# Performance work log

Hardware: AMD Instinct MI355X
Metric: run time of the kernel (lower is better)

Reference implementation:

```python
import jax, jax.numpy as jnp
import numpy as np

D = 1024
H = 16
DH = D // H  # 64
EPS = 1e-6


def setup_inputs() -> dict:
    key = jax.random.key(0)
    ks = jax.random.split(key, 12)
    B, Nq, Nk = 4, 2048, 2048
    s = 1.0 / np.sqrt(D)
    return {
        "x": jax.random.normal(ks[0], (B, Nq, D), dtype=jnp.float32),
        "context": jax.random.normal(ks[1], (B, Nk, D), dtype=jnp.float32),
        "Wq": jax.random.normal(ks[2], (D, D), dtype=jnp.float32) * s,
        "bq": jnp.zeros((D,), dtype=jnp.float32),
        "Wk": jax.random.normal(ks[3], (D, D), dtype=jnp.float32) * s,
        "bk": jnp.zeros((D,), dtype=jnp.float32),
        "Wv": jax.random.normal(ks[4], (D, D), dtype=jnp.float32) * s,
        "bv": jnp.zeros((D,), dtype=jnp.float32),
        "Wo": jax.random.normal(ks[5], (D, D), dtype=jnp.float32) * s,
        "bo": jnp.zeros((D,), dtype=jnp.float32),
    }


def _split_heads(t):
    B, N, _ = t.shape
    return t.reshape(B, N, H, DH).transpose(0, 2, 1, 3)  # (B,H,N,DH)


def reference(x, context, Wq, bq, Wk, bk, Wv, bv, Wo, bo):
    B, Nq, _ = x.shape
    # QKV projections (torch Linear: x @ W.T + b)
    q = _split_heads(x @ Wq.T + bq)          # (B,H,Nq,DH)
    k = _split_heads(context @ Wk.T + bk)    # (B,H,Nk,DH)
    v = _split_heads(context @ Wv.T + bv)    # (B,H,Nk,DH)
    # QK-norm (use_qk_norm=True), scale buffer = 1.0
    q = q / (jnp.linalg.norm(q, axis=-1, keepdims=True) + EPS)
    k = k / (jnp.linalg.norm(k, axis=-1, keepdims=True) + EPS)
    scale = jnp.float32(1.0)
    attn = jnp.einsum("bhqd,bhkd->bhqk", q, k) * scale
    attn = jax.nn.softmax(attn, axis=-1)
    out = jnp.einsum("bhqk,bhkd->bhqd", attn, v)  # (B,H,Nq,DH)
    out = out.transpose(0, 2, 1, 3).reshape(B, Nq, D)
    return out @ Wo.T + bo
```

## Files before the change

### kernel.cpp

```cpp
#include <hip/hip_runtime.h>

typedef unsigned short u16;
typedef unsigned int u32;
typedef __attribute__((ext_vector_type(8))) short bf16x8;
typedef __attribute__((ext_vector_type(4))) float f32x4;
typedef __attribute__((ext_vector_type(16))) float f32x16;
typedef __attribute__((ext_vector_type(4))) u32 u32x4;

#define D_MODEL 1024
#define NHEAD 16
#define DHEAD 64
#define SEQ 2048
#define BATCH 4
#define MTOT (BATCH * SEQ)
#define LOG2E 1.4426950408889634f

#define MFMA16(A, B, C) __builtin_amdgcn_mfma_f32_16x16x32_bf16((A), (B), (C), 0, 0, 0)
#define MFMA32(A, B, C) __builtin_amdgcn_mfma_f32_32x32x16_bf16((A), (B), (C), 0, 0, 0)

__device__ __forceinline__ u16 f2bf(float f) {
  u32 u = __builtin_bit_cast(u32, f);
  u = (u + 0x7FFFu + ((u >> 16) & 1u)) >> 16;
  return (u16)u;
}

__device__ __forceinline__ void async_copy16(void* lds, const void* g) {
  __builtin_amdgcn_global_load_lds(
      (const __attribute__((address_space(1))) u32*)g,
      (__attribute__((address_space(3))) u32*)lds, 16, 0, 0);
}

__device__ __forceinline__ u32 cvtpk_bf16(float lo, float hi) {
  u32 r;
  asm("v_cvt_pk_bf16_f32 %0, %1, %2" : "=v"(r) : "v"(lo), "v"(hi));
  return r;
}
__device__ __forceinline__ void permswap(u32& a, u32& b) {
  asm("v_permlane32_swap_b32 %0, %1" : "+v"(a), "+v"(b));
}

__device__ __forceinline__ void wg_barrier() {
  __builtin_amdgcn_sched_barrier(0);
  asm volatile("s_barrier" ::: "memory");
  __builtin_amdgcn_sched_barrier(0);
}
#define VMCNT(N) asm volatile("s_waitcnt vmcnt(" #N ")" ::: "memory")

__global__ void cvt_all(const float* __restrict__ x, const float* __restrict__ ctx,
                        const float* __restrict__ Wq, const float* __restrict__ Wk,
                        const float* __restrict__ Wv, const float* __restrict__ Wo,
                        u16* __restrict__ xb, u16* __restrict__ cb,
                        u16* __restrict__ wqb, u16* __restrict__ wkb,
                        u16* __restrict__ wvb, u16* __restrict__ wob) {
  const int NX = 1 << 21;
  const int NW = 1 << 18;
  const int total = 2 * NX + 4 * NW;
  int i = blockIdx.x * blockDim.x + threadIdx.x;
  const int st = gridDim.x * blockDim.x;
  for (; i < total; i += st) {
    const float* s; u16* d; int j;
    if (i < NX)            { s = x;   d = xb;  j = i; }
    else if (i < 2 * NX)   { s = ctx; d = cb;  j = i - NX; }
    else {
      int k = i - 2 * NX;
      int wi = k >> 18;
      j = k & (NW - 1);
      s = (wi == 0) ? Wq : (wi == 1) ? Wk : (wi == 2) ? Wv : Wo;
      d = (wi == 0) ? wqb : (wi == 1) ? wkb : (wi == 2) ? wvb : wob;
    }
    float4 v = ((const float4*)s)[j];
    ushort4 o;
    o.x = f2bf(v.x); o.y = f2bf(v.y); o.z = f2bf(v.z); o.w = f2bf(v.w);
    ((ushort4*)d)[j] = o;
  }
}

__global__ __launch_bounds__(256, 3) void gemm_qkv(
    const u16* __restrict__ xb, const u16* __restrict__ cb,
    const u16* __restrict__ wqb, const u16* __restrict__ wkvb,
    const float* __restrict__ bq, const float* __restrict__ bk,
    const float* __restrict__ bv,
    u16* __restrict__ Qb, u16* __restrict__ Kb, u16* __restrict__ Vtb) {
  __shared__ u16 As[128 * 64];
  __shared__ u16 Bs[128 * 64];
  const int K = 1024;
  const int tid = threadIdx.x;
  const int l = tid & 63;
  const int wid = tid >> 6;
  const int bid = blockIdx.x;
  const int swz = (bid & 7) * 192 + (bid >> 3);
  const bool isQ = swz < 512;
  const u16* A;
  const u16* Bw;
  int m0, n0;
  if (isQ) {
    A = xb; Bw = wqb;
    m0 = (swz >> 3) * 128;
    n0 = (swz & 7) * 128;
  } else {
    const int s = swz - 512;
    A = cb; Bw = wkvb;
    m0 = (s >> 4) * 128;
    n0 = (s & 15) * 128;
  }
  const int wr = wid >> 1, wc = wid & 1;
  const int r = l & 15, kg = l >> 4;
  f32x4 acc[4][4] = {};
  char* AsB = (char*)As;
  char* BsB = (char*)Bs;
  const int arow = l >> 3;
  const int agran = (l & 7) ^ arow;

  for (int kt = 0; kt < K; kt += 64) {
#pragma unroll
    for (int cc = 0; cc < 4; ++cc) {
      int c = wid + (cc << 2);
      int rowi = (c << 3) + arow;
      const char* ga = (const char*)A + ((size_t)(m0 + rowi) * K + kt) * 2 + agran * 16;
      async_copy16(AsB + c * 1024, ga);
      const char* gb = (const char*)Bw + ((size_t)(n0 + rowi) * K + kt) * 2 + agran * 16;
      async_copy16(BsB + c * 1024, gb);
    }
    __syncthreads();
#pragma unroll
    for (int half = 0; half < 2; ++half) {
      const int g = ((half << 2) + kg) ^ (r & 7);
      bf16x8 af[4], bf[4];
#pragma unroll
      for (int i = 0; i < 4; ++i) {
        af[i] = *(const bf16x8*)(AsB + (wr * 64 + i * 16 + r) * 128 + g * 16);
        bf[i] = *(const bf16x8*)(BsB + (wc * 64 + i * 16 + r) * 128 + g * 16);
      }
#pragma unroll
      for (int i = 0; i < 4; ++i)
#pragma unroll
        for (int j = 0; j < 4; ++j)
          acc[i][j] = MFMA16(af[i], bf[j], acc[i][j]);
    }
    __syncthreads();
  }

  const int colbase = n0 + wc * 64;
  const bool isV = (!isQ) && (colbase >= 1024);
  if (!isV) {
    u16* C = isQ ? Qb : Kb;
    const float* bias = isQ ? bq : bk;
    const float sMul = isQ ? LOG2E : 1.0f;
    float bvj[4];
#pragma unroll
    for (int j = 0; j < 4; ++j) bvj[j] = bias[colbase + j * 16 + r];
#pragma unroll
    for (int i = 0; i < 4; ++i) {
      const int row0 = m0 + wr * 64 + i * 16 + kg * 4;
#pragma unroll
      for (int jj = 0; jj < 4; ++jj) {
        float t[4];
        float s2 = 0.f;
#pragma unroll
        for (int j = 0; j < 4; ++j) {
          t[j] = acc[i][j][jj] + bvj[j];
          s2 += t[j] * t[j];
        }
        s2 += __shfl_xor(s2, 1);
        s2 += __shfl_xor(s2, 2);
        s2 += __shfl_xor(s2, 4);
        s2 += __shfl_xor(s2, 8);
        const float inv = sMul / (sqrtf(s2) + 1e-6f);
#pragma unroll
        for (int j = 0; j < 4; ++j)
          C[(size_t)(row0 + jj) * D_MODEL + colbase + j * 16 + r] = f2bf(t[j] * inv);
      }
    }
  } else {
#pragma unroll
    for (int i = 0; i < 4; ++i) {
#pragma unroll
      for (int j = 0; j < 4; ++j) {
        const int col = colbase + j * 16 + r;
        const float bvv = bv[col - 1024];
        const int row0 = m0 + wr * 64 + i * 16 + kg * 4;
        const int hh = (col - 1024) >> 6, dh = col & 63;
        const int bb = row0 >> 11, tok = row0 & 2047;
        ushort4 o;
        o.x = f2bf(acc[i][j][0] + bvv);
        o.y = f2bf(acc[i][j][1] + bvv);
        o.z = f2bf(acc[i][j][2] + bvv);
        o.w = f2bf(acc[i][j][3] + bvv);
        *(ushort4*)(Vtb + ((size_t)((bb * 16 + hh) * 64 + dh) * SEQ + tok)) = o;
      }
    }
  }
}

__global__ __launch_bounds__(256, 3) void gemm_out(const u16* __restrict__ A,
                                                   const u16* __restrict__ Bw,
                                                   const float* __restrict__ bias,
                                                   float* __restrict__ Cout) {
  __shared__ u16 As[128 * 64];
  __shared__ u16 Bs[128 * 64];
  const int K = 1024, N = 1024;
  const int tid = threadIdx.x;
  const int l = tid & 63;
  const int wid = tid >> 6;
  const int bid = blockIdx.x;
  const int swz = (bid & 7) * 64 + (bid >> 3);
  const int m0 = (swz >> 3) * 128;
  const int n0 = (swz & 7) * 128;
  const int wr = wid >> 1, wc = wid & 1;
  const int r = l & 15, kg = l >> 4;
  f32x4 acc[4][4] = {};
  char* AsB = (char*)As;
  char* BsB = (char*)Bs;
  const int arow = l >> 3;
  const int agran = (l & 7) ^ arow;

  for (int kt = 0; kt < K; kt += 64) {
#pragma unroll
    for (int cc = 0; cc < 4; ++cc) {
      int c = wid + (cc << 2);
      int rowi = (c << 3) + arow;
      const char* ga = (const char*)A + ((size_t)(m0 + rowi) * K + kt) * 2 + agran * 16;
      async_copy16(AsB + c * 1024, ga);
      const char* gb = (const char*)Bw + ((size_t)(n0 + rowi) * K + kt) * 2 + agran * 16;
      async_copy16(BsB + c * 1024, gb);
    }
    __syncthreads();
#pragma unroll
    for (int half = 0; half < 2; ++half) {
      const int g = ((half << 2) + kg) ^ (r & 7);
      bf16x8 af[4], bf[4];
#pragma unroll
      for (int i = 0; i < 4; ++i) {
        af[i] = *(const bf16x8*)(AsB + (wr * 64 + i * 16 + r) * 128 + g * 16);
        bf[i] = *(const bf16x8*)(BsB + (wc * 64 + i * 16 + r) * 128 + g * 16);
      }
#pragma unroll
      for (int i = 0; i < 4; ++i)
#pragma unroll
        for (int j = 0; j < 4; ++j)
          acc[i][j] = MFMA16(af[i], bf[j], acc[i][j]);
    }
    __syncthreads();
  }
#pragma unroll
  for (int i = 0; i < 4; ++i) {
#pragma unroll
    for (int j = 0; j < 4; ++j) {
      const int col = n0 + wc * 64 + j * 16 + r;
      const float bvv = bias[col];
      const int row0 = m0 + wr * 64 + i * 16 + kg * 4;
#pragma unroll
      for (int jj = 0; jj < 4; ++jj)
        Cout[(size_t)(row0 + jj) * N + col] = acc[i][j][jj] + bvv;
    }
  }
}

#define KVB 64
#define NT (SEQ / KVB)

__global__ __launch_bounds__(256, 4) void attn_kernel(const u16* __restrict__ Q,
                                                      const u16* __restrict__ K,
                                                      const u16* __restrict__ Vt,
                                                      u16* __restrict__ O) {
  __shared__ alignas(16) u16 Ks[2][KVB * 64];
  __shared__ alignas(16) u16 Vs[2][64 * KVB];
  const int tid = threadIdx.x;
  const int l = tid & 63;
  const int wid = tid >> 6;
  const int qg = l & 31;
  const int half = l >> 5;
  const int bid = blockIdx.x;
  const int swz = (bid & 7) * 128 + (bid >> 3);
  const int qt = swz & 15;
  const int bh = swz >> 4;
  const int b = bh >> 4, h = bh & 15;

  const int srow = l >> 3, slot = l & 7;
  const int r0 = (wid << 3) + srow;
  const int r1 = ((wid + 4) << 3) + srow;
  const int sw0 = (r0 ^ (r0 >> 3)) & 7;
  const int sw1 = (r1 ^ (r1 >> 3)) & 7;
  const u16* pK0 = K + ((size_t)(b * SEQ) + r0) * D_MODEL + h * 64 + (slot ^ sw0) * 8;
  const u16* pK1 = K + ((size_t)(b * SEQ) + r1) * D_MODEL + h * 64 + (slot ^ sw1) * 8;
  const u16* pV0 = Vt + ((size_t)(bh * 64) + r0) * SEQ + (slot ^ sw0) * 8;
  const u16* pV1 = Vt + ((size_t)(bh * 64) + r1) * SEQ + (slot ^ sw1) * 8;
  const int ldsc0 = wid * 1024, ldsc1 = (wid + 4) * 1024;

  bf16x8 qf[4];
  {
    const u16* q0 = Q + ((size_t)(b * SEQ + qt * 128 + wid * 32 + qg)) * D_MODEL + h * 64 + half * 8;
#pragma unroll
    for (int dc = 0; dc < 4; ++dc) qf[dc] = *(const bf16x8*)(q0 + dc * 16);
  }
  f32x16 oacc[2] = {};
  float lrun = 0.f;

  auto stage = [&](int bufi) {
    char* KsX = (char*)Ks[bufi];
    char* VsX = (char*)Vs[bufi];
    async_copy16(KsX + ldsc0, pK0);
    async_copy16(KsX + ldsc1, pK1);
    async_copy16(VsX + ldsc0, pV0);
    async_copy16(VsX + ldsc1, pV1);
    pK0 += (size_t)KVB * D_MODEL;
    pK1 += (size_t)KVB * D_MODEL;
    pV0 += KVB;
    pV1 += KVB;
  };

  auto process = [&](int bufi) {
    const char* KsC = (const char*)Ks[bufi];
    const char* VsC = (const char*)Vs[bufi];
    f32x16 st[2] = {};
    __builtin_amdgcn_s_setprio(1);
#pragma unroll
    for (int t32 = 0; t32 < 2; ++t32) {
      const int rowK = t32 * 32 + qg;
      const int swk = (rowK ^ (rowK >> 3)) & 7;
#pragma unroll
      for (int dc = 0; dc < 4; ++dc) {
        const int p = (dc * 2 + half) ^ swk;
        bf16x8 kf = *(const bf16x8*)(KsC + rowK * 128 + p * 16);
        st[t32] = MFMA32(kf, qf[dc], st[t32]);
      }
    }
    __builtin_amdgcn_s_setprio(0);

    float rs0 = 0.f, rs1 = 0.f, rs2 = 0.f, rs3 = 0.f;
#pragma unroll
    for (int t32 = 0; t32 < 2; ++t32)
#pragma unroll
      for (int rr = 0; rr < 16; rr += 4) {
        float p0 = __builtin_amdgcn_exp2f(st[t32][rr + 0]);
        float p1 = __builtin_amdgcn_exp2f(st[t32][rr + 1]);
        float p2 = __builtin_amdgcn_exp2f(st[t32][rr + 2]);
        float p3 = __builtin_amdgcn_exp2f(st[t32][rr + 3]);
        st[t32][rr + 0] = p0; st[t32][rr + 1] = p1;
        st[t32][rr + 2] = p2; st[t32][rr + 3] = p3;
        rs0 += p0; rs1 += p1; rs2 += p2; rs3 += p3;
      }
    lrun += (rs0 + rs1) + (rs2 + rs3);

#pragma unroll
    for (int t32 = 0; t32 < 2; ++t32) {
#pragma unroll
      for (int cc = 0; cc < 2; ++cc) {
        const int base = cc * 8;
        u32 wA = cvtpk_bf16(st[t32][base + 0], st[t32][base + 1]);
        u32 wB = cvtpk_bf16(st[t32][base + 2], st[t32][base + 3]);
        u32 wC = cvtpk_bf16(st[t32][base + 4], st[t32][base + 5]);
        u32 wD = cvtpk_bf16(st[t32][base + 6], st[t32][base + 7]);
        permswap(wA, wC);
        permswap(wB, wD);
        u32x4 pw = {wA, wB, wC, wD};
        bf16x8 pf = __builtin_bit_cast(bf16x8, pw);
        const int qw = ((t32 * 2 + cc) << 1) + half;
        __builtin_amdgcn_s_setprio(1);
#pragma unroll
        for (int dt = 0; dt < 2; ++dt) {
          const int rowV = dt * 32 + qg;
          const int pp = qw ^ ((rowV ^ (rowV >> 3)) & 7);
          bf16x8 vf = *(const bf16x8*)(VsC + rowV * 128 + pp * 16);
          oacc[dt] = MFMA32(vf, pf, oacc[dt]);
        }
        __builtin_amdgcn_s_setprio(0);
      }
    }
  };

  stage(0);
  stage(1);
  VMCNT(0);
  wg_barrier();

  for (int t = 0; t < NT - 1; ++t) {
    VMCNT(4);
    wg_barrier();
    process(t & 1);
    wg_barrier();
    if (t + 2 < NT) stage(t & 1);
  }
  VMCNT(0);
  wg_barrier();
  process((NT - 1) & 1);

  lrun += __shfl_xor(lrun, 32);
  const float inv = 1.0f / lrun;
  u32* orow = (u32*)(O + ((size_t)(b * SEQ + qt * 128 + wid * 32 + qg)) * D_MODEL + h * 64);
#pragma unroll
  for (int dt = 0; dt < 2; ++dt)
#pragma unroll
    for (int w = 0; w < 8; ++w) {
      const int dh = dt * 32 + (w & 1) * 2 + 8 * (w >> 1) + 4 * half;
      u32 pk = cvtpk_bf16(oacc[dt][2 * w] * inv, oacc[dt][2 * w + 1] * inv);
      orow[dh >> 1] = pk;
    }
}

extern "C" void kernel_launch(void* const* d_in, const int* in_sizes, int n_in,
                              void* d_out, int out_size, void* d_ws, size_t ws_size,
                              hipStream_t stream) {
  const float* x   = (const float*)d_in[0];
  const float* ctx = (const float*)d_in[1];
  const float* Wq  = (const float*)d_in[2];
  const float* bq  = (const float*)d_in[3];
  const float* Wk  = (const float*)d_in[4];
  const float* bk  = (const float*)d_in[5];
  const float* Wv  = (const float*)d_in[6];
  const float* bv  = (const float*)d_in[7];
  const float* Wo  = (const float*)d_in[8];
  const float* bo  = (const float*)d_in[9];
  float* out = (float*)d_out;

  const size_t NTOK = (size_t)MTOT * D_MODEL;
  const size_t WSZ = (size_t)D_MODEL * D_MODEL;
  u16* xb  = (u16*)d_ws;
  u16* cb  = xb + NTOK;
  u16* wqb = cb + NTOK;
  u16* wkb = wqb + WSZ;
  u16* wvb = wkb + WSZ;
  u16* wob = wvb + WSZ;
  u16* Qb  = wob + WSZ;
  u16* Kb  = Qb + NTOK;
  u16* Vtb = Kb + NTOK;
  (void)in_sizes; (void)n_in; (void)out_size; (void)ws_size;

  dim3 blk(256);
  cvt_all<<<2048, blk, 0, stream>>>(x, ctx, Wq, Wk, Wv, Wo, xb, cb, wqb, wkb, wvb, wob);

  gemm_qkv<<<1536, blk, 0, stream>>>(xb, cb, wqb, wkb, bq, bk, bv, Qb, Kb, Vtb);

  attn_kernel<<<1024, blk, 0, stream>>>(Qb, Kb, Vtb, xb);

  gemm_out<<<512, blk, 0, stream>>>(xb, wob, bo, out);
}
```

Measured before the change: 178.7 us.

## Store V in MFMA-fragment layout and load it directly from global memory

The QKV GEMM now writes V in a pre-swizzled fragment order, so each lane's bf16x8 operand for the PV MFMA is contiguous. The attention kernel drops the shared-memory V buffer and loads V fragments straight from global (L2) into registers each tile, issued early to overlap with the exp step. K staging is restructured so the refill of the freed buffer starts mid-iteration. The aim is to cut LDS traffic, LDS capacity and async-copy work per tile, in exchange for more global loads with latency exposed on the critical path and more registers held per lane.

```diff
diff --git a/kernel.cpp b/kernel.cpp
--- a/kernel.cpp
+++ b/kernel.cpp
@@ -80,7 +80,7 @@
     const u16* __restrict__ wqb, const u16* __restrict__ wkvb,
     const float* __restrict__ bq, const float* __restrict__ bk,
     const float* __restrict__ bv,
-    u16* __restrict__ Qb, u16* __restrict__ Kb, u16* __restrict__ Vtb) {
+    u16* __restrict__ Qb, u16* __restrict__ Kb, u16* __restrict__ Vfb) {
   __shared__ u16 As[128 * 64];
   __shared__ u16 Bs[128 * 64];
   const int K = 1024;
@@ -179,14 +179,18 @@
         const int col = colbase + j * 16 + r;
         const float bvv = bv[col - 1024];
         const int row0 = m0 + wr * 64 + i * 16 + kg * 4;
-        const int hh = (col - 1024) >> 6, dh = col & 63;
+        const int dh = col & 63;
         const int bb = row0 >> 11, tok = row0 & 2047;
+        const int bh2 = bb * 16 + ((col - 1024) >> 6);
         ushort4 o;
         o.x = f2bf(acc[i][j][0] + bvv);
         o.y = f2bf(acc[i][j][1] + bvv);
         o.z = f2bf(acc[i][j][2] + bvv);
         o.w = f2bf(acc[i][j][3] + bvv);
-        *(ushort4*)(Vtb + ((size_t)((bb * 16 + hh) * 64 + dh) * SEQ + tok)) = o;
+        const size_t off =
+            ((size_t)(bh2 * 32 + (tok >> 6)) * 8 + ((tok >> 4) & 3) * 2 + (dh >> 5)) * 512 +
+            ((dh & 31) + ((tok >> 3) & 1) * 32) * 8 + (tok & 7);
+        *(ushort4*)(Vfb + off) = o;
       }
     }
   }
@@ -261,10 +265,9 @@
 
 __global__ __launch_bounds__(256, 4) void attn_kernel(const u16* __restrict__ Q,
                                                       const u16* __restrict__ K,
-                                                      const u16* __restrict__ Vt,
+                                                      const u16* __restrict__ Vf,
                                                       u16* __restrict__ O) {
   __shared__ alignas(16) u16 Ks[2][KVB * 64];
-  __shared__ alignas(16) u16 Vs[2][64 * KVB];
   const int tid = threadIdx.x;
   const int l = tid & 63;
   const int wid = tid >> 6;
@@ -283,9 +286,8 @@
   const int sw1 = (r1 ^ (r1 >> 3)) & 7;
   const u16* pK0 = K + ((size_t)(b * SEQ) + r0) * D_MODEL + h * 64 + (slot ^ sw0) * 8;
   const u16* pK1 = K + ((size_t)(b * SEQ) + r1) * D_MODEL + h * 64 + (slot ^ sw1) * 8;
-  const u16* pV0 = Vt + ((size_t)(bh * 64) + r0) * SEQ + (slot ^ sw0) * 8;
-  const u16* pV1 = Vt + ((size_t)(bh * 64) + r1) * SEQ + (slot ^ sw1) * 8;
   const int ldsc0 = wid * 1024, ldsc1 = (wid + 4) * 1024;
+  const u16* pV = Vf + (size_t)bh * 32 * 8 * 512 + l * 8;
 
   bf16x8 qf[4];
   {
@@ -296,22 +298,22 @@
   f32x16 oacc[2] = {};
   float lrun = 0.f;
 
-  auto stage = [&](int bufi) {
+  auto stageK = [&](int bufi) {
     char* KsX = (char*)Ks[bufi];
-    char* VsX = (char*)Vs[bufi];
     async_copy16(KsX + ldsc0, pK0);
     async_copy16(KsX + ldsc1, pK1);
-    async_copy16(VsX + ldsc0, pV0);
-    async_copy16(VsX + ldsc1, pV1);
     pK0 += (size_t)KVB * D_MODEL;
     pK1 += (size_t)KVB * D_MODEL;
-    pV0 += KVB;
-    pV1 += KVB;
   };
 
-  auto process = [&](int bufi) {
-    const char* KsC = (const char*)Ks[bufi];
-    const char* VsC = (const char*)Vs[bufi];
+  stageK(0);
+  stageK(1);
+  VMCNT(2);
+  wg_barrier();
+
+  for (int t = 0; t < NT; ++t) {
+    const char* KsC = (const char*)Ks[t & 1];
+
     f32x16 st[2] = {};
     __builtin_amdgcn_s_setprio(1);
 #pragma unroll
@@ -326,6 +328,16 @@
       }
     }
     __builtin_amdgcn_s_setprio(0);
+
+    bf16x8 vf[4][2];
+    {
+      const u16* vt = pV + (size_t)t * 4096;
+#pragma unroll
+      for (int sl = 0; sl < 4; ++sl) {
+        vf[sl][0] = *(const bf16x8*)(vt + sl * 1024);
+        vf[sl][1] = *(const bf16x8*)(vt + sl * 1024 + 512);
+      }
+    }
 
     float rs0 = 0.f, rs1 = 0.f, rs2 = 0.f, rs3 = 0.f;
 #pragma unroll
@@ -341,6 +353,9 @@
         rs0 += p0; rs1 += p1; rs2 += p2; rs3 += p3;
       }
     lrun += (rs0 + rs1) + (rs2 + rs3);
+
+    wg_barrier();
+    if (t + 2 < NT) stageK(t & 1);
 
 #pragma unroll
     for (int t32 = 0; t32 < 2; ++t32) {
@@ -355,35 +370,16 @@
         permswap(wB, wD);
         u32x4 pw = {wA, wB, wC, wD};
         bf16x8 pf = __builtin_bit_cast(bf16x8, pw);
-        const int qw = ((t32 * 2 + cc) << 1) + half;
+        const int sl = t32 * 2 + cc;
         __builtin_amdgcn_s_setprio(1);
-#pragma unroll
-        for (int dt = 0; dt < 2; ++dt) {
-          const int rowV = dt * 32 + qg;
-          const int pp = qw ^ ((rowV ^ (rowV >> 3)) & 7);
-          bf16x8 vf = *(const bf16x8*)(VsC + rowV * 128 + pp * 16);
-          oacc[dt] = MFMA32(vf, pf, oacc[dt]);
-        }
+        oacc[0] = MFMA32(vf[sl][0], pf, oacc[0]);
+        oacc[1] = MFMA32(vf[sl][1], pf, oacc[1]);
         __builtin_amdgcn_s_setprio(0);
       }
     }
-  };
-
-  stage(0);
-  stage(1);
-  VMCNT(0);
-  wg_barrier();
-
-  for (int t = 0; t < NT - 1; ++t) {
-    VMCNT(4);
+    VMCNT(2);
     wg_barrier();
-    process(t & 1);
-    wg_barrier();
-    if (t + 2 < NT) stage(t & 1);
-  }
-  VMCNT(0);
-  wg_barrier();
-  process((NT - 1) & 1);
+  }
 
   lrun += __shfl_xor(lrun, 32);
   const float inv = 1.0f / lrun;
@@ -423,15 +419,15 @@
   u16* wob = wvb + WSZ;
   u16* Qb  = wob + WSZ;
   u16* Kb  = Qb + NTOK;
-  u16* Vtb = Kb + NTOK;
+  u16* Vfb = Kb + NTOK;
   (void)in_sizes; (void)n_in; (void)out_size; (void)ws_size;
 
   dim3 blk(256);
   cvt_all<<<2048, blk, 0, stream>>>(x, ctx, Wq, Wk, Wv, Wo, xb, cb, wqb, wkb, wvb, wob);
 
-  gemm_qkv<<<1536, blk, 0, stream>>>(xb, cb, wqb, wkb, bq, bk, bv, Qb, Kb, Vtb);
-
-  attn_kernel<<<1024, blk, 0, stream>>>(Qb, Kb, Vtb, xb);
+  gemm_qkv<<<1536, blk, 0, stream>>>(xb, cb, wqb, wkb, bq, bk, bv, Qb, Kb, Vfb);
+
+  attn_kernel<<<1024, blk, 0, stream>>>(Qb, Kb, Vfb, xb);
 
   gemm_out<<<512, blk, 0, stream>>>(xb, wob, bo, out);
 }
```

Measured after the change: 193.6 us. 1.08x slower.
